# Kernel optimization log

Measured on AMD Instinct MI355X. Metric: run time of the kernel, lower is better.

The kernel has to match this reference:

```python
import jax, jax.numpy as jnp
import numpy as np
import math

EMB_IN = 512
EMB_OUT = 512
HEADS = 8
MAX_LEN = 5000


def _pe_matrix(max_len, d_model):
    pos = np.arange(max_len, dtype=np.float32)[:, None]
    div = np.exp(np.arange(0, d_model, 2, dtype=np.float32) * (-math.log(10000.0) / d_model))
    pe = np.zeros((max_len, d_model), dtype=np.float32)
    pe[:, 0::2] = np.sin(pos * div)
    pe[:, 1::2] = np.cos(pos * div)
    return jnp.asarray(pe)


def setup_inputs() -> dict:
    key = jax.random.key(0)
    ks = jax.random.split(key, 8)
    b, t = 16, 512
    e_in, e, h = EMB_IN, EMB_OUT, HEADS
    # xavier-ish scales
    def xn(k, shape):
        fan_in, fan_out = shape[0], shape[-1]
        std = math.sqrt(2.0 / (fan_in + fan_out))
        return jax.random.normal(k, shape, dtype=jnp.float32) * std
    return {
        "x": jax.random.normal(ks[0], (b, t, e_in), dtype=jnp.float32),
        "W_proj": xn(ks[1], (e_in, e)),           # projection (no bias)
        "W_k": xn(ks[2], (e, h * e)),
        "W_q": xn(ks[3], (e, h * e)),
        "W_v": xn(ks[4], (e, h * e)),
        "W_unify": xn(ks[5], (h * e, e)),
        "b_unify": jnp.zeros((e,), dtype=jnp.float32),
        "query": xn(ks[6], (e, 1)),               # attention-pooling query
    }


def reference(x, W_proj, W_k, W_q, W_v, W_unify, b_unify, query):
    b, t, _ = x.shape
    h, e = HEADS, EMB_OUT
    pe = _pe_matrix(MAX_LEN, e)  # constant, no grad
    # linear projection + positional encoding
    x = x @ W_proj + pe[:t][None]                      # [b,t,e]
    # multi-head attention (per-head dim == e)
    scale = e ** (-0.25)
    q = (x @ W_q).reshape(b, t, h, e) * scale
    k = (x @ W_k).reshape(b, t, h, e) * scale
    v = (x @ W_v).reshape(b, t, h, e)
    dot = jnp.einsum('bthe,bshe->bhts', q, k)          # [b,h,t,t]
    att = jax.nn.softmax(dot, axis=-1)
    out = jnp.einsum('bhts,bshe->bthe', att, v).reshape(b, t, h * e)
    out = out @ W_unify + b_unify                      # [b,t,e]
    # attention pooling
    pool_scores = jax.nn.softmax((out @ query)[..., 0], axis=1)  # [b,t]
    pooled = jnp.einsum('bt,bte->be', pool_scores, out)          # [b,e]
    return pooled
```

## Files before the change

kernel.cpp:

```cpp
#include <hip/hip_runtime.h>
#include <hip/hip_bf16.h>

typedef unsigned short u16;
typedef u16   u16x4  __attribute__((ext_vector_type(4)));
typedef u16   u16x8  __attribute__((ext_vector_type(8)));
typedef float f32x16 __attribute__((ext_vector_type(16)));


__device__ __forceinline__ u16 f2bf(float f) {
    union { float f; unsigned u; } v; v.f = f;
    unsigned u = v.u;
    unsigned r = (u + 0x7fffu + ((u >> 16) & 1u)) >> 16;
    return (u16)r;
}
__device__ __forceinline__ float bf2f(u16 u) {
    union { unsigned u; float f; } x; x.u = (unsigned)u << 16; return x.f;
}

__device__ __forceinline__ void mfma32(f32x16& d, u16x8 a, u16x8 b) {
    asm("v_mfma_f32_32x32x16_bf16 %0, %1, %2, %0" : "+v"(d) : "v"(a), "v"(b));
}


#define LDK 72

template<int EPI, int SWZ = 0, bool AF32 = false, int SPLITZ = 0>
__global__ __launch_bounds__(256)
void gemm_bt(const void* __restrict__ Av, const u16* __restrict__ BT,
             void* __restrict__ Cv, const float* __restrict__ aux,
             int lda, int ldb, int K, long sAb, long sBb, int z0,
             const void* __restrict__ Av2, void* __restrict__ Cv2, int z1)
{
    __shared__ u16 smem[2][128 * LDK];
    u16* As = smem[0];
    u16* Bs = smem[1];

    const int tid  = threadIdx.x;
    const int lane = tid & 63;
    const int wid  = tid >> 6;
    const int wm   = wid >> 1, wn = wid & 1;
    const int bz   = blockIdx.z;

    int bx = blockIdx.x, by = blockIdx.y;
    if (SWZ == 1) {
        const int gx = gridDim.x;
        const int n  = gx * gridDim.y;
        const int q  = n >> 3;
        int f = by * gx + bx;
        f = (f & 7) * q + (f >> 3);
        bx = f % gx; by = f / gx;
    } else if (SWZ == 2) {
        const int orig = by * gridDim.x + bx;
        const int xcd  = orig & 7;
        const int j    = orig >> 3;
        const int s    = xcd + ((j >> 6) << 3);
        const int t    = j & 63;
        bx = ((s & 7) << 3) + (t & 7);
        by = ((s >> 3) << 3) + (t >> 3);
    }
    const int m0 = bx * 128;
    const int n0 = by * 128;

    const u16* Ab;
    const float* Af = (const float*)Av + (size_t)bz * sAb;
    if (SPLITZ == 2 && bz >= z1)
        Ab = (const u16*)Av2 + (size_t)(bz - z1) * sAb;
    else
        Ab = (const u16*)Av + (size_t)bz * sAb;
    const u16* Bb = BT + (size_t)bz * sBb;

    u16* Cb = (u16*)Cv;
    int bzc = bz;
    if (SPLITZ == 1 && bz >= z1) { Cb = (u16*)Cv2; bzc = bz - z1; }

    const int tr = tid >> 3;
    const int tc = (tid & 7) << 3;

    f32x16 acc[2][2];
#pragma unroll
    for (int i = 0; i < 2; ++i)
#pragma unroll
        for (int j = 0; j < 2; ++j)
            acc[i][j] = (f32x16){0.f,0.f,0.f,0.f,0.f,0.f,0.f,0.f,
                                 0.f,0.f,0.f,0.f,0.f,0.f,0.f,0.f};

    asm volatile("s_nop 3"
        : "+v"(acc[0][0]), "+v"(acc[0][1]), "+v"(acc[1][0]), "+v"(acc[1][1]));

    const int fr = lane & 31;
    const int q8 = (lane >> 5) << 3;

    for (int kt = 0; kt < K; kt += 64) {
        __syncthreads();
#pragma unroll
        for (int j = 0; j < 4; ++j) {
            const int r = tr + 32 * j;
            if (AF32) {
                const float* pa = &Af[(size_t)(m0 + r) * lda + kt + tc];
                float4 f0 = *(const float4*)pa;
                float4 f1 = *(const float4*)(pa + 4);
                u16x8 w = { f2bf(f0.x), f2bf(f0.y), f2bf(f0.z), f2bf(f0.w),
                            f2bf(f1.x), f2bf(f1.y), f2bf(f1.z), f2bf(f1.w) };
                *(u16x8*)&As[r * LDK + tc] = w;
            } else {
                *(u16x8*)&As[r * LDK + tc] = *(const u16x8*)&Ab[(size_t)(m0 + r) * lda + kt + tc];
            }
            *(u16x8*)&Bs[r * LDK + tc] = *(const u16x8*)&Bb[(size_t)(n0 + r) * ldb + kt + tc];
        }
        __syncthreads();

#pragma unroll
        for (int ks = 0; ks < 4; ++ks) {
            const int ko = ks * 16 + q8;
            u16x8 a0 = *(const u16x8*)&As[(wm * 64 +      fr) * LDK + ko];
            u16x8 a1 = *(const u16x8*)&As[(wm * 64 + 32 + fr) * LDK + ko];
            u16x8 b0 = *(const u16x8*)&Bs[(wn * 64 +      fr) * LDK + ko];
            u16x8 b1 = *(const u16x8*)&Bs[(wn * 64 + 32 + fr) * LDK + ko];
            mfma32(acc[0][0], a0, b0);
            mfma32(acc[0][1], a0, b1);
            mfma32(acc[1][0], a1, b0);
            mfma32(acc[1][1], a1, b1);
        }
    }

    asm volatile("s_nop 7\n\ts_nop 7\n\ts_nop 7"
        : "+v"(acc[0][0]), "+v"(acc[0][1]), "+v"(acc[1][0]), "+v"(acc[1][1]));

    const int lc = lane & 31;
    const int lq = (lane >> 5) << 2;

    if (EPI == 7) {
#pragma unroll
        for (int mi = 0; mi < 2; ++mi)
#pragma unroll
            for (int ni = 0; ni < 2; ++ni)
#pragma unroll
                for (int i = 0; i < 16; ++i) {
                    const int row = m0 + wm * 64 + mi * 32 + (i & 3) + 8 * (i >> 2) + lq;
                    const int col = n0 + wn * 64 + ni * 32 + lc;
                    ((float*)Cv)[((size_t)bz << 22) + (size_t)row * 512 + col] = acc[mi][ni][i];
                }
        return;
    }

    u16* cs = (u16*)smem;
    auto cswz = [](int r, int c) { return r * 128 + (c ^ (((r >> 3) & 7) << 4)); };
    __syncthreads();
#pragma unroll
    for (int mi = 0; mi < 2; ++mi)
#pragma unroll
        for (int ni = 0; ni < 2; ++ni)
#pragma unroll
            for (int i = 0; i < 16; ++i) {
                const int rl = wm * 64 + mi * 32 + (i & 3) + 8 * (i >> 2) + lq;
                const int cl = wn * 64 + ni * 32 + lc;
                float v = acc[mi][ni][i];
                if (EPI == 0) v += aux[(((m0 + rl) & 511) << 9) + n0 + cl];
                cs[cswz(rl, cl)] = f2bf(v);
            }
    __syncthreads();

    if (EPI == 5 && n0 >= 8192) {
        const int elq = tid >> 4;
        const int t8  = (tid & 15) << 3;
        const int hh  = (n0 >> 9) & 7;
        const int bb  = m0 >> 9;
        const int e0v = n0 & 511;
        const int t0v = m0 & 511;
        u16* Vbase = (u16*)Cv + 67108864;
#pragma unroll
        for (int q = 0; q < 8; ++q) {
            const int e_loc = q * 16 + elq;
            u16x8 w;
#pragma unroll
            for (int k = 0; k < 8; ++k) w[k] = cs[cswz(t8 + k, e_loc)];
            const size_t dst = ((size_t)(hh * 16 + bb) << 18)
                             + (size_t)(e0v + e_loc) * 512 + t0v + t8;
            *(u16x8*)&Vbase[dst] = w;
        }
        return;
    }

    const int frl = tid >> 4;
    const int fc8 = (tid & 15) << 3;
#pragma unroll
    for (int p = 0; p < 8; ++p) {
        const int rl = p * 16 + frl;
        u16x8 w = *(u16x8*)&cs[rl * 128 + (fc8 ^ (((rl >> 3) & 7) << 4))];
        const int row = m0 + rl;
        const int col = n0 + fc8;
        size_t dst;
        u16* dstp;
        if (EPI == 0) {
            dst = (size_t)row * 512 + col;
            dstp = (u16*)Cv;
        } else if (EPI == 3) {
            dst = ((size_t)bzc << 18) + ((size_t)row << 9) + col;
            dstp = Cb;
        } else if (EPI == 5) {
            const int part = col >> 12;
            const int h    = (col >> 9) & 7;
            const int e    = col & 511;
            dst = ((size_t)(part * 8 + h) * 8192 + row) * 512 + e;
            dstp = (u16*)Cv;
        } else {
            const int zz = bz + z0;
            const int bb = zz & 15;
            const int hh = zz >> 4;
            dst = ((size_t)(bb * 512 + row)) * 4096 + hh * 512 + col;
            dstp = (u16*)Cv;
        }
        *(u16x8*)&dstp[dst] = w;
    }
}


__global__ __launch_bounds__(256)
void transpose_cast(const float* __restrict__ in, u16* __restrict__ out, int R, int C) {
    __shared__ float t[32][33];
    const int tx = threadIdx.x & 31, ty = threadIdx.x >> 5;
    const int c0 = blockIdx.x * 32, r0 = blockIdx.y * 32;
#pragma unroll
    for (int j = 0; j < 4; ++j)
        t[ty + 8 * j][tx] = in[(size_t)(r0 + ty + 8 * j) * C + c0 + tx];
    __syncthreads();
#pragma unroll
    for (int j = 0; j < 4; ++j)
        out[(size_t)(c0 + ty + 8 * j) * R + r0 + tx] = f2bf(t[tx][ty + 8 * j]);
}

__global__ __launch_bounds__(256)
void transpose_cast3(const float* __restrict__ a, const float* __restrict__ b,
                     const float* __restrict__ c, u16* __restrict__ out) {
    const float* in = blockIdx.z == 0 ? a : (blockIdx.z == 1 ? b : c);
    u16* o = out + (size_t)blockIdx.z * 2097152;
    __shared__ float t[32][33];
    const int tx = threadIdx.x & 31, ty = threadIdx.x >> 5;
    const int c0 = blockIdx.x * 32, r0 = blockIdx.y * 32;
#pragma unroll
    for (int j = 0; j < 4; ++j)
        t[ty + 8 * j][tx] = in[(size_t)(r0 + ty + 8 * j) * 4096 + c0 + tx];
    __syncthreads();
#pragma unroll
    for (int j = 0; j < 4; ++j)
        o[(size_t)(c0 + ty + 8 * j) * 512 + r0 + tx] = f2bf(t[tx][ty + 8 * j]);
}

__global__ __launch_bounds__(256)
void pe_fill(float* __restrict__ pe) {
    const int idx = blockIdx.x * 256 + threadIdx.x;
    const int p = idx >> 8, i2 = idx & 255;
    const float div = expf((float)(2 * i2) * -0.017988946039015984f);
    const float arg = (float)p * div;
    pe[(p << 9) + 2 * i2]     = sinf(arg);
    pe[(p << 9) + 2 * i2 + 1] = cosf(arg);
}

__global__ __launch_bounds__(256)
void diag_fill(float* __restrict__ out, int n, float val) {
    const int i = blockIdx.x * 256 + threadIdx.x;
    if (i < n) out[i] = val;
}

__global__ __launch_bounds__(64)
void softmax_bf16(u16* __restrict__ S1, u16* __restrict__ S2, int n1) {
    const size_t row = blockIdx.x;
    u16* p = (row < (size_t)n1 ? S1 + (row << 9) : S2 + ((row - n1) << 9))
           + threadIdx.x * 8;
    u16x8 w = *(u16x8*)p;
    float v[8];
#pragma unroll
    for (int j = 0; j < 8; ++j) v[j] = bf2f(w[j]);
    float m = fmaxf(fmaxf(fmaxf(v[0], v[1]), fmaxf(v[2], v[3])),
                    fmaxf(fmaxf(v[4], v[5]), fmaxf(v[6], v[7])));
#pragma unroll
    for (int o = 32; o > 0; o >>= 1) m = fmaxf(m, __shfl_xor(m, o, 64));
    const float lam = 0.044194173824159216f;
    float s = 0.f;
#pragma unroll
    for (int j = 0; j < 8; ++j) { v[j] = __expf((v[j] - m) * lam); s += v[j]; }
#pragma unroll
    for (int o = 32; o > 0; o >>= 1) s += __shfl_xor(s, o, 64);
    const float inv = 1.0f / s;
#pragma unroll
    for (int j = 0; j < 8; ++j) w[j] = f2bf(v[j] * inv);
    *(u16x8*)p = w;
}

__global__ __launch_bounds__(256)
void combine_dot(const float* __restrict__ pk, const float* __restrict__ bu,
                 const float* __restrict__ qry, float* __restrict__ outb,
                 float* __restrict__ sc) {
    const int row = blockIdx.x, t = threadIdx.x;
    const size_t b0 = (size_t)row * 512;
    float o0 = pk[b0 + t]       + pk[b0 + t + 4194304]       + bu[t];
    float o1 = pk[b0 + t + 256] + pk[b0 + t + 256 + 4194304] + bu[t + 256];
    outb[b0 + t]       = o0;
    outb[b0 + t + 256] = o1;
    float acc = o0 * qry[t] + o1 * qry[t + 256];
    const int lane = t & 63, wid = t >> 6;
    __shared__ float red[4];
#pragma unroll
    for (int o = 32; o > 0; o >>= 1) acc += __shfl_xor(acc, o, 64);
    if (lane == 0) red[wid] = acc;
    __syncthreads();
    if (t == 0) sc[row] = red[0] + red[1] + red[2] + red[3];
}

__global__ __launch_bounds__(256)
void pool_softmax(const float* __restrict__ sc, float* __restrict__ p) {
    const int b = blockIdx.x, tid = threadIdx.x;
    const int lane = tid & 63, wid = tid >> 6;
    __shared__ float red[8];
    float v0 = sc[(b << 9) + tid];
    float v1 = sc[(b << 9) + 256 + tid];
    float m = fmaxf(v0, v1);
#pragma unroll
    for (int o = 32; o > 0; o >>= 1) m = fmaxf(m, __shfl_xor(m, o, 64));
    if (lane == 0) red[wid] = m;
    __syncthreads();
    m = fmaxf(fmaxf(red[0], red[1]), fmaxf(red[2], red[3]));
    float e0 = __expf(v0 - m), e1 = __expf(v1 - m);
    float s = e0 + e1;
#pragma unroll
    for (int o = 32; o > 0; o >>= 1) s += __shfl_xor(s, o, 64);
    if (lane == 0) red[4 + wid] = s;
    __syncthreads();
    s = red[4] + red[5] + red[6] + red[7];
    const float inv = 1.0f / s;
    p[(b << 9) + tid]       = e0 * inv;
    p[(b << 9) + 256 + tid] = e1 * inv;
}

__global__ __launch_bounds__(512)
void pool_partial(const float* __restrict__ outb, const float* __restrict__ p,
                  float* __restrict__ part) {
    const int ts = blockIdx.x, b = blockIdx.y, e = threadIdx.x;
    float acc = 0.f;
#pragma unroll 8
    for (int tt = 0; tt < 64; ++tt) {
        const int t = ts * 64 + tt;
        acc += p[(b << 9) + t] * outb[((size_t)(b * 512 + t) << 9) + e];
    }
    part[((size_t)(ts * 16 + b) << 9) + e] = acc;
}

__global__ __launch_bounds__(256)
void pool_reduce(const float* __restrict__ part, float* __restrict__ dout) {
    const int i = blockIdx.x * 256 + threadIdx.x;
    const int b = i >> 9, e = i & 511;
    float acc = 0.f;
#pragma unroll
    for (int ts = 0; ts < 8; ++ts) acc += part[((size_t)(ts * 16 + b) << 9) + e];
    dout[i] = acc;
}


extern "C" void kernel_launch(void* const* d_in, const int* in_sizes, int n_in,
                              void* d_out, int out_size, void* d_ws, size_t ws_size,
                              hipStream_t stream)
{
    (void)in_sizes; (void)n_in;
    const float* x   = (const float*)d_in[0];
    const float* Wp  = (const float*)d_in[1];
    const float* Wk  = (const float*)d_in[2];
    const float* Wq  = (const float*)d_in[3];
    const float* Wv  = (const float*)d_in[4];
    const float* Wu  = (const float*)d_in[5];
    const float* bu  = (const float*)d_in[6];
    const float* qry = (const float*)d_in[7];

    char* ws = (char*)d_ws;
    const size_t NEED = 268435456ull;
    if (ws_size < NEED) {
        diag_fill<<<(out_size + 255) / 256, 256, 0, stream>>>(
            (float*)d_out, out_size, (float)(ws_size >> 20));
        return;
    }

    u16*   WpT   = (u16*)(ws + 0);
    u16*   WqT   = (u16*)(ws + 524288);
    float* peb   = (float*)(ws + 13107200);
    u16*   Xp    = (u16*)(ws + 14155776);
    u16*   QKV   = (u16*)(ws + 22544384);
    u16*   Qb    = QKV;
    u16*   Kb    = (u16*)(ws + 89653248);
    u16*   Vt    = (u16*)(ws + 156762112);
    u16*   S1    = (u16*)(ws + 0);
    u16*   S2    = (u16*)(ws + 223870976);
    u16*   Ob    = (u16*)(ws + 22544384);
    float* partK = (float*)(ws + 89653248);
    float* outb  = (float*)(ws + 123207680);
    u16*   WuT   = (u16*)(ws + 0);
    float* scb   = (float*)(ws + 22544384);
    float* poolp = (float*)(ws + 22577152);
    float* pbf   = (float*)(ws + 22839296);

    transpose_cast<<<dim3(16, 16), 256, 0, stream>>>(Wp, WpT, 512, 512);
    transpose_cast3<<<dim3(128, 16, 3), 256, 0, stream>>>(Wq, Wk, Wv, WqT);
    pe_fill<<<512, 256, 0, stream>>>(peb);

    gemm_bt<0, 1, true><<<dim3(64, 4, 1), 256, 0, stream>>>(
        x, WpT, Xp, peb, 512, 512, 512, 0, 0, 0, nullptr, nullptr, 0);
    gemm_bt<5, 2><<<dim3(64, 96, 1), 256, 0, stream>>>(
        Xp, WqT, QKV, nullptr, 512, 512, 512, 0, 0, 0, nullptr, nullptr, 0);

    gemm_bt<3, 0, false, 1><<<dim3(4, 4, 128), 256, 0, stream>>>(
        Qb, Kb, S1, nullptr, 512, 512, 512, 262144, 262144, 0, nullptr, S2, 43);

    softmax_bf16<<<65536, 64, 0, stream>>>(S1, S2, 22016);

    gemm_bt<6, 0, false, 2><<<dim3(4, 4, 128), 256, 0, stream>>>(
        S1, Vt, Ob, nullptr, 512, 512, 512, 262144, 262144, 0, S2, nullptr, 43);

    transpose_cast<<<dim3(16, 128), 256, 0, stream>>>(Wu, WuT, 4096, 512);

    gemm_bt<7, 1><<<dim3(64, 4, 2), 256, 0, stream>>>(
        Ob, WuT, partK, nullptr, 4096, 4096, 2048, 2048, 2048, 0, nullptr, nullptr, 0);
    combine_dot<<<8192, 256, 0, stream>>>(partK, bu, qry, outb, scb);

    pool_softmax<<<16, 256, 0, stream>>>(scb, pbf);
    pool_partial<<<dim3(8, 16), 512, 0, stream>>>(outb, pbf, poolp);
    pool_reduce<<<32, 256, 0, stream>>>(poolp, (float*)d_out);
}
```

Baseline: 415.4 us.

## Fold Wq·Wkᵀ into per-head bilinear matrix instead of materialising Q and K

```diff
diff --git a/kernel.cpp b/kernel.cpp
--- a/kernel.cpp
+++ b/kernel.cpp
@@ -24,12 +24,11 @@
 
 #define LDK 72
 
-template<int EPI, int SWZ = 0, bool AF32 = false, int SPLITZ = 0>
+template<int EPI, int SWZ = 0, bool AF32 = false, int ASEL = 0, int BSEL = 0>
 __global__ __launch_bounds__(256)
 void gemm_bt(const void* __restrict__ Av, const u16* __restrict__ BT,
              void* __restrict__ Cv, const float* __restrict__ aux,
-             int lda, int ldb, int K, long sAb, long sBb, int z0,
-             const void* __restrict__ Av2, void* __restrict__ Cv2, int z1)
+             int lda, int ldb, int K, long sAb, long sBb)
 {
     __shared__ u16 smem[2][128 * LDK];
     u16* As = smem[0];
@@ -61,17 +60,11 @@
     const int m0 = bx * 128;
     const int n0 = by * 128;
 
-    const u16* Ab;
-    const float* Af = (const float*)Av + (size_t)bz * sAb;
-    if (SPLITZ == 2 && bz >= z1)
-        Ab = (const u16*)Av2 + (size_t)(bz - z1) * sAb;
-    else
-        Ab = (const u16*)Av + (size_t)bz * sAb;
-    const u16* Bb = BT + (size_t)bz * sBb;
-
-    u16* Cb = (u16*)Cv;
-    int bzc = bz;
-    if (SPLITZ == 1 && bz >= z1) { Cb = (u16*)Cv2; bzc = bz - z1; }
+    const long az = (ASEL == 0) ? bz : (bz >> 3);
+    const long bzb = (BSEL == 0) ? bz : (BSEL == 1 ? (bz >> 3) : (bz & 7));
+    const u16*   Ab = (const u16*)Av   + az * sAb;
+    const float* Af = (const float*)Av + az * sAb;
+    const u16*   Bb = BT + bzb * sBb;
 
     const int tr = tid >> 3;
     const int tc = (tid & 7) << 3;
@@ -160,23 +153,22 @@
             }
     __syncthreads();
 
-    if (EPI == 5 && n0 >= 8192) {
+    if (EPI == 8) {
         const int elq = tid >> 4;
         const int t8  = (tid & 15) << 3;
-        const int hh  = (n0 >> 9) & 7;
+        const int hh  = n0 >> 9;
         const int bb  = m0 >> 9;
         const int e0v = n0 & 511;
         const int t0v = m0 & 511;
-        u16* Vbase = (u16*)Cv + 67108864;
 #pragma unroll
         for (int q = 0; q < 8; ++q) {
             const int e_loc = q * 16 + elq;
             u16x8 w;
 #pragma unroll
             for (int k = 0; k < 8; ++k) w[k] = cs[cswz(t8 + k, e_loc)];
-            const size_t dst = ((size_t)(hh * 16 + bb) << 18)
+            const size_t dst = ((size_t)(bb * 8 + hh) << 18)
                              + (size_t)(e0v + e_loc) * 512 + t0v + t8;
-            *(u16x8*)&Vbase[dst] = w;
+            *(u16x8*)&((u16*)Cv)[dst] = w;
         }
         return;
     }
@@ -190,27 +182,16 @@
         const int row = m0 + rl;
         const int col = n0 + fc8;
         size_t dst;
-        u16* dstp;
         if (EPI == 0) {
             dst = (size_t)row * 512 + col;
-            dstp = (u16*)Cv;
         } else if (EPI == 3) {
-            dst = ((size_t)bzc << 18) + ((size_t)row << 9) + col;
-            dstp = Cb;
-        } else if (EPI == 5) {
-            const int part = col >> 12;
-            const int h    = (col >> 9) & 7;
-            const int e    = col & 511;
-            dst = ((size_t)(part * 8 + h) * 8192 + row) * 512 + e;
-            dstp = (u16*)Cv;
+            dst = ((size_t)bz << 18) + ((size_t)row << 9) + col;
         } else {
-            const int zz = bz + z0;
-            const int bb = zz & 15;
-            const int hh = zz >> 4;
+            const int bb = bz >> 3;
+            const int hh = bz & 7;
             dst = ((size_t)(bb * 512 + row)) * 4096 + hh * 512 + col;
-            dstp = (u16*)Cv;
         }
-        *(u16x8*)&dstp[dst] = w;
+        *(u16x8*)&((u16*)Cv)[dst] = w;
     }
 }
 
@@ -230,20 +211,14 @@
 }
 
 __global__ __launch_bounds__(256)
-void transpose_cast3(const float* __restrict__ a, const float* __restrict__ b,
-                     const float* __restrict__ c, u16* __restrict__ out) {
-    const float* in = blockIdx.z == 0 ? a : (blockIdx.z == 1 ? b : c);
-    u16* o = out + (size_t)blockIdx.z * 2097152;
-    __shared__ float t[32][33];
-    const int tx = threadIdx.x & 31, ty = threadIdx.x >> 5;
-    const int c0 = blockIdx.x * 32, r0 = blockIdx.y * 32;
-#pragma unroll
-    for (int j = 0; j < 4; ++j)
-        t[ty + 8 * j][tx] = in[(size_t)(r0 + ty + 8 * j) * 4096 + c0 + tx];
-    __syncthreads();
-#pragma unroll
-    for (int j = 0; j < 4; ++j)
-        o[(size_t)(c0 + ty + 8 * j) * 512 + r0 + tx] = f2bf(t[tx][ty + 8 * j]);
+void cast2(const float* __restrict__ a, const float* __restrict__ b,
+           u16* __restrict__ oa, u16* __restrict__ ob) {
+    const float* in = blockIdx.z == 0 ? a : b;
+    u16* o = blockIdx.z == 0 ? oa : ob;
+    const int i = blockIdx.x * 256 + threadIdx.x;
+    float4 v = ((const float4*)in)[i];
+    u16x4 w = { f2bf(v.x), f2bf(v.y), f2bf(v.z), f2bf(v.w) };
+    ((u16x4*)o)[i] = w;
 }
 
 __global__ __launch_bounds__(256)
@@ -262,11 +237,11 @@
     if (i < n) out[i] = val;
 }
 
-__global__ __launch_bounds__(64)
-void softmax_bf16(u16* __restrict__ S1, u16* __restrict__ S2, int n1) {
-    const size_t row = blockIdx.x;
-    u16* p = (row < (size_t)n1 ? S1 + (row << 9) : S2 + ((row - n1) << 9))
-           + threadIdx.x * 8;
+__global__ __launch_bounds__(256)
+void softmax_bf16(u16* __restrict__ S) {
+    const size_t row = (size_t)blockIdx.x * 4 + (threadIdx.x >> 6);
+    const int lane = threadIdx.x & 63;
+    u16* p = S + (row << 9) + lane * 8;
     u16x8 w = *(u16x8*)p;
     float v[8];
 #pragma unroll
@@ -371,7 +346,7 @@
     const float* qry = (const float*)d_in[7];
 
     char* ws = (char*)d_ws;
-    const size_t NEED = 268435456ull;
+    const size_t NEED = 261619712ull;
     if (ws_size < NEED) {
         diag_fill<<<(out_size + 255) / 256, 256, 0, stream>>>(
             (float*)d_out, out_size, (float)(ws_size >> 20));
@@ -379,44 +354,52 @@
     }
 
     u16*   WpT   = (u16*)(ws + 0);
-    u16*   WqT   = (u16*)(ws + 524288);
+    u16*   WqC   = (u16*)(ws + 524288);
+    u16*   WkC   = (u16*)(ws + 4718592);
+    u16*   Mbuf  = (u16*)(ws + 8912896);
     float* peb   = (float*)(ws + 13107200);
     u16*   Xp    = (u16*)(ws + 14155776);
-    u16*   QKV   = (u16*)(ws + 22544384);
-    u16*   Qb    = QKV;
-    u16*   Kb    = (u16*)(ws + 89653248);
-    u16*   Vt    = (u16*)(ws + 156762112);
-    u16*   S1    = (u16*)(ws + 0);
-    u16*   S2    = (u16*)(ws + 223870976);
-    u16*   Ob    = (u16*)(ws + 22544384);
-    float* partK = (float*)(ws + 89653248);
-    float* outb  = (float*)(ws + 123207680);
-    u16*   WuT   = (u16*)(ws + 0);
-    float* scb   = (float*)(ws + 22544384);
-    float* poolp = (float*)(ws + 22577152);
-    float* pbf   = (float*)(ws + 22839296);
+    u16*   WvT   = (u16*)(ws + 22544384);
+    u16*   Tb    = (u16*)(ws + 26738688);
+    u16*   Ob    = (u16*)(ws + 26738688);
+    u16*   Vt    = (u16*)(ws + 93847552);
+    u16*   WuT   = (u16*)(ws + 93847552);
+    u16*   Sb    = (u16*)(ws + 160956416);
+    float* outb  = (float*)(ws + 160956416);
+    float* scb   = (float*)(ws + 177733632);
+    float* poolp = (float*)(ws + 177766400);
+    float* pbf   = (float*)(ws + 178028544);
+    float* partK = (float*)(ws + 228065280);
 
     transpose_cast<<<dim3(16, 16), 256, 0, stream>>>(Wp, WpT, 512, 512);
-    transpose_cast3<<<dim3(128, 16, 3), 256, 0, stream>>>(Wq, Wk, Wv, WqT);
+    transpose_cast<<<dim3(128, 16), 256, 0, stream>>>(Wv, WvT, 512, 4096);
+    cast2<<<dim3(2048, 1, 2), 256, 0, stream>>>(Wq, Wk, WqC, WkC);
     pe_fill<<<512, 256, 0, stream>>>(peb);
 
     gemm_bt<0, 1, true><<<dim3(64, 4, 1), 256, 0, stream>>>(
-        x, WpT, Xp, peb, 512, 512, 512, 0, 0, 0, nullptr, nullptr, 0);
-    gemm_bt<5, 2><<<dim3(64, 96, 1), 256, 0, stream>>>(
-        Xp, WqT, QKV, nullptr, 512, 512, 512, 0, 0, 0, nullptr, nullptr, 0);
-
-    gemm_bt<3, 0, false, 1><<<dim3(4, 4, 128), 256, 0, stream>>>(
-        Qb, Kb, S1, nullptr, 512, 512, 512, 262144, 262144, 0, nullptr, S2, 43);
-
-    softmax_bf16<<<65536, 64, 0, stream>>>(S1, S2, 22016);
-
-    gemm_bt<6, 0, false, 2><<<dim3(4, 4, 128), 256, 0, stream>>>(
-        S1, Vt, Ob, nullptr, 512, 512, 512, 262144, 262144, 0, S2, nullptr, 43);
+        x, WpT, Xp, peb, 512, 512, 512, 0, 0);
+
+    gemm_bt<3><<<dim3(4, 4, 8), 256, 0, stream>>>(
+        WkC, WqC, Mbuf, nullptr, 4096, 4096, 512, 512, 512);
+
+    gemm_bt<8, 2><<<dim3(64, 32, 1), 256, 0, stream>>>(
+        Xp, WvT, Vt, nullptr, 512, 512, 512, 0, 0);
+
+    gemm_bt<3, 0, false, 1, 2><<<dim3(4, 4, 128), 256, 0, stream>>>(
+        Xp, Mbuf, Tb, nullptr, 512, 512, 512, 262144, 262144);
+
+    gemm_bt<3, 0, false, 0, 1><<<dim3(4, 4, 128), 256, 0, stream>>>(
+        Tb, Xp, Sb, nullptr, 512, 512, 512, 262144, 262144);
+
+    softmax_bf16<<<16384, 256, 0, stream>>>(Sb);
+
+    gemm_bt<6><<<dim3(4, 4, 128), 256, 0, stream>>>(
+        Sb, Vt, Ob, nullptr, 512, 512, 512, 262144, 262144);
 
     transpose_cast<<<dim3(16, 128), 256, 0, stream>>>(Wu, WuT, 4096, 512);
 
     gemm_bt<7, 1><<<dim3(64, 4, 2), 256, 0, stream>>>(
-        Ob, WuT, partK, nullptr, 4096, 4096, 2048, 2048, 2048, 0, nullptr, nullptr, 0);
+        Ob, WuT, partK, nullptr, 4096, 4096, 2048, 2048, 2048);
     combine_dot<<<8192, 256, 0, stream>>>(partK, bu, qry, outb, scb);
 
     pool_softmax<<<16, 256, 0, stream>>>(scb, pbf);
```

Result: faster. 375.4 us, median of 2 (-9.6%).
